# Kernel optimization log

Hardware: AMD Instinct MI355X
Metric: run time of the kernel (lower is better)

Reference implementation:

```python
import jax, jax.numpy as jnp
import numpy as np

N_NODES = 100000
N_EDGES = 2000000


def _init_mlp(key, dims, scale=0.05):
    Ws, bs = [], []
    ks = jax.random.split(key, len(dims) - 1)
    for k, di, do in zip(ks, dims[:-1], dims[1:]):
        Ws.append(jax.random.normal(k, (di, do), dtype=jnp.float32) * scale)
        bs.append(jnp.zeros((do,), dtype=jnp.float32))
    return Ws, bs


def setup_inputs() -> dict:
    key = jax.random.key(0)
    ks = jax.random.split(key, 7)
    d = {
        "t": jax.random.uniform(ks[0], (1,), dtype=jnp.float32),
        "x": jax.random.normal(ks[1], (N_NODES, 4), dtype=jnp.float32),
        "Ofixed": jax.random.normal(ks[2], (N_NODES, 2), dtype=jnp.float32),
        "src_idx": jax.random.randint(ks[3], (N_EDGES,), 0, N_NODES, dtype=jnp.int32),
        "tgt_idx": jax.random.randint(ks[4], (N_EDGES,), 0, N_NODES, dtype=jnp.int32),
    }
    # fR: (2*d_O+1)=13 -> [150]*4 -> 50 ; fO: 50 -> [100] -> 4
    R_Ws, R_bs = _init_mlp(ks[5], [13, 150, 150, 150, 150, 50])
    O_Ws, O_bs = _init_mlp(ks[6], [50, 100, 4])
    for i, (W, b) in enumerate(zip(R_Ws, R_bs)):
        d[f"fR_W{i}"] = W
        d[f"fR_b{i}"] = b
    for i, (W, b) in enumerate(zip(O_Ws, O_bs)):
        d[f"fO_W{i}"] = W
        d[f"fO_b{i}"] = b
    return d


def _mlp(h, Ws, bs):
    # hidden layers with ReLU, linear output (matches MLP in the torch code)
    for W, b in zip(Ws[:-1], bs[:-1]):
        h = jax.nn.relu(h @ W + b)
    return h @ Ws[-1] + bs[-1]


def reference(t, x, Ofixed, src_idx, tgt_idx,
              fR_W0, fR_b0, fR_W1, fR_b1, fR_W2, fR_b2, fR_W3, fR_b3, fR_W4, fR_b4,
              fO_W0, fO_b0, fO_W1, fO_b1):
    O = jnp.concatenate([x, Ofixed], axis=1)            # [N, d_O]
    # Msrc.T @ O and Mtgt.T @ O with 0/1 incidence matrices == gathers
    Rsrc = O[src_idx]                                   # [M, d_O]
    Rtgt = O[tgt_idx]                                   # [M, d_O]
    tt = jnp.broadcast_to(t.reshape(1, 1).astype(O.dtype), (src_idx.shape[0], 1))
    R_prime = jnp.concatenate([Rsrc, Rtgt, tt], axis=1)  # [M, 2*d_O+1]
    E = _mlp(R_prime, [fR_W0, fR_W1, fR_W2, fR_W3, fR_W4],
             [fR_b0, fR_b1, fR_b2, fR_b3, fR_b4])        # [M, d_E]
    # Mtgt @ E == scatter-add of edge messages onto target nodes
    E_prime = jax.ops.segment_sum(E, tgt_idx, num_segments=x.shape[0])  # [N, d_E]
    P = _mlp(E_prime, [fO_W0, fO_W1], [fO_b0, fO_b1])    # [N, d_P]
    return P
```

## Files before the change

### kernel.cpp

```cpp
#include <hip/hip_runtime.h>
#include <hip/hip_bf16.h>

typedef unsigned short u16;
typedef unsigned int u32;
typedef __attribute__((ext_vector_type(8))) short short8;
typedef __attribute__((ext_vector_type(4))) float f32x4;

constexpr int SA     = 160;
constexpr int BLK_E  = 128;
constexpr int NTHR   = 256;
constexpr int CHUNK  = 512;
constexpr int WSLOT  = 50 * CHUNK;
constexpr size_t WS_HDR   = 262144;

constexpr int Ls (int s) { return s == 0 ? 0 : (s <= 15 ? 1 + (s - 1) / 5 : 4); }
constexpr int Kss(int s) { return s == 0 ? 0 : (s <= 15 ? (s - 1) % 5 : s - 16); }

__device__ __forceinline__ u16 f2bf(float f) {
    union { float f; unsigned u; } c; c.f = f;
    return (u16)((c.u + 0x7fffu + ((c.u >> 16) & 1u)) >> 16);
}
__device__ __forceinline__ unsigned pk_bf16(float a, float b) {
    float2 f; f.x = a; f.y = b;
    __hip_bfloat162 h = __float22bfloat162_rn(f);
    return *(unsigned*)&h;
}

__device__ __forceinline__ int kperm(int kp) {
    if (kp < 64)  return (kp & 3) * 16 + (kp >> 2);
    if (kp < 128) { const int m = kp - 64; return (5 + (m & 3)) * 16 + (m >> 2); }
    if (kp < 144) return 4 * 16 + (kp - 128);
    if (kp < 160) return 9 * 16 + (kp - 144);
    return 1 << 30;
}

__global__ void prep_all(const float* __restrict__ W0, const float* __restrict__ W1,
                         const float* __restrict__ W2, const float* __restrict__ W3,
                         const float* __restrict__ W4,
                         const float* __restrict__ B0, const float* __restrict__ B1,
                         const float* __restrict__ B2, const float* __restrict__ B3,
                         const float* __restrict__ B4,
                         u16* __restrict__ Wt, u32* __restrict__ cursor, int n_nodes)
{
    const int l = blockIdx.y;
    if (l == 5) {
        for (int idx = blockIdx.x * blockDim.x + threadIdx.x; idx < n_nodes;
             idx += gridDim.x * blockDim.x)
            cursor[idx] = 0u;
        return;
    }
    const float* W; const float* B; int DI, DO; bool perm;
    if      (l == 0) { W = W0; B = B0; DI = 13;  DO = 150; perm = false; }
    else if (l == 1) { W = W1; B = B1; DI = 150; DO = 150; perm = true;  }
    else if (l == 2) { W = W2; B = B2; DI = 150; DO = 150; perm = true;  }
    else if (l == 3) { W = W3; B = B3; DI = 150; DO = 150; perm = true;  }
    else             { W = W4; B = B4; DI = 150; DO = 50;  perm = true;  }
    const int kbias = (l == 0) ? 13 : 150;
    u16* dst = Wt + (size_t)l * WSLOT;
    for (int idx = blockIdx.x * blockDim.x + threadIdx.x; idx < WSLOT;
         idx += gridDim.x * blockDim.x) {
        const int chunk = idx / CHUNK;
        const int within = idx - chunk * CHUNK;
        const int lane = within >> 3, e = within & 7;
        const int ks = chunk / 10, j = chunk - ks * 10;
        const int c = lane & 15, q = lane >> 4;
        const int n = j * 16 + c;
        const int kphys = ks * 32 + q * 8 + e;
        const int klog = perm ? kperm(kphys) : kphys;
        float v = 0.f;
        if (n < DO) {
            if (klog < DI)          v = W[klog * DO + n];
            else if (klog == kbias) v = B[n];
        }
        dst[idx] = f2bf(v);
    }
}

__device__ __forceinline__ void loadHalfH(const u16* __restrict__ Wt, int h,
                                          int lane, short8* buf)
{
    int l, ks, g, nch;
    if (h < 32) { const int s = h >> 1; l = Ls(s); ks = Kss(s); g = h & 1; nch = 5; }
    else        { l = 4; ks = h - 32; g = 0; nch = 4; }
    const u16* base = Wt + (size_t)l * WSLOT + (size_t)(ks * 10 + g * 5) * CHUNK
                         + lane * 8;
#pragma unroll
    for (int jj = 0; jj < 5; ++jj)
        if (jj < nch) buf[jj] = *(const short8*)&base[jj * CHUNK];
}

__device__ __forceinline__ void epilogueF(u16* act, int ebase, int col, int quad,
                                          f32x4 (&acc)[2][10])
{
#pragma unroll
    for (int mtl = 0; mtl < 2; ++mtl)
#pragma unroll
        for (int r = 0; r < 4; ++r) {
            const int row = ebase + mtl * 16 + quad * 4 + r;
            u16* rp = &act[row * SA];
            uint2 p0, p1;
            p0.x = pk_bf16(fmaxf(acc[mtl][0][r], 0.f), fmaxf(acc[mtl][1][r], 0.f));
            p0.y = pk_bf16(fmaxf(acc[mtl][2][r], 0.f), fmaxf(acc[mtl][3][r], 0.f));
            p1.x = pk_bf16(fmaxf(acc[mtl][5][r], 0.f), fmaxf(acc[mtl][6][r], 0.f));
            p1.y = pk_bf16(fmaxf(acc[mtl][7][r], 0.f), fmaxf(acc[mtl][8][r], 0.f));
            *(uint2*)&rp[col * 4]      = p0;
            *(uint2*)&rp[64 + col * 4] = p1;
            rp[128 + col] = (u16)pk_bf16(fmaxf(acc[mtl][4][r], 0.f), 0.f);
            u16 sv = (u16)pk_bf16(fmaxf(acc[mtl][9][r], 0.f), 0.f);
            if (col == 6) sv = 0x3F80;
            rp[144 + col] = sv;
        }
}

__global__ void hist_kernel(const int* __restrict__ tgt, u32* __restrict__ cnt,
                            int n_edges)
{
    const int e = blockIdx.x * blockDim.x + threadIdx.x;
    if (e < n_edges) atomicAdd(&cnt[tgt[e]], 1u);
}

__global__ void scan1_kernel(const u32* __restrict__ cnt, u32* __restrict__ offs,
                             u32* __restrict__ bsum, int n)
{
    __shared__ u32 s[256];
    const int i = blockIdx.x * 256 + threadIdx.x;
    const u32 v = (i < n) ? cnt[i] : 0u;
    s[threadIdx.x] = v; __syncthreads();
#pragma unroll
    for (int d = 1; d < 256; d <<= 1) {
        const u32 t = (threadIdx.x >= d) ? s[threadIdx.x - d] : 0u;
        __syncthreads();
        s[threadIdx.x] += t;
        __syncthreads();
    }
    if (i < n) offs[i] = s[threadIdx.x] - v;
    if (threadIdx.x == 255) bsum[blockIdx.x] = s[255];
}

__global__ void scan2_kernel(u32* __restrict__ bsum, int nb)
{
    __shared__ u32 s[512];
    const int i = threadIdx.x;
    const u32 v = (i < nb) ? bsum[i] : 0u;
    s[i] = v; __syncthreads();
#pragma unroll
    for (int d = 1; d < 512; d <<= 1) {
        const u32 t = (i >= d) ? s[i - d] : 0u;
        __syncthreads();
        s[i] += t;
        __syncthreads();
    }
    if (i < nb) bsum[i] = s[i] - v;
}

__global__ void scan3_kernel(u32* __restrict__ offs, const u32* __restrict__ bsum,
                             u32* __restrict__ cursor, int n, int n_edges)
{
    const int i = blockIdx.x * 256 + threadIdx.x;
    if (i < n) {
        const u32 o = offs[i] + bsum[blockIdx.x];
        offs[i] = o;
        cursor[i] = o;
    }
    if (blockIdx.x == 0 && threadIdx.x == 0) offs[n] = (u32)n_edges;
}

__global__ void perm_kernel(const int* __restrict__ src, const int* __restrict__ tgt,
                            u32* __restrict__ cursor, int2* __restrict__ sg,
                            int n_edges)
{
    const int e = blockIdx.x * blockDim.x + threadIdx.x;
    if (e < n_edges) {
        const int g = tgt[e];
        const u32 pos = atomicAdd(&cursor[g], 1u);
        sg[pos] = make_int2(src[e], g);
    }
}

__global__ __launch_bounds__(NTHR, 3) void edge_kernel(
    const float* __restrict__ t, const float* __restrict__ x, const float* __restrict__ Ofx,
    const int2* __restrict__ sgp,
    const u16* __restrict__ Wt,
    float* __restrict__ Ep, int n_edges)
{
    __shared__ __align__(16) u16 act[BLK_E * SA];

    const int tid   = threadIdx.x;
    const int lane  = tid & 63;
    const int wv    = tid >> 6;
    const int ebase = wv * 32;
    const int col   = lane & 15;
    const int quad  = lane >> 4;

    int gval = -1;
    if (lane < 32) {
        const int e = ebase + lane;
        const long long ge = (long long)blockIdx.x * BLK_E + e;
        const bool valid = ge < n_edges;
        const int2 sg = valid ? sgp[ge] : make_int2(0, 0);
        gval = valid ? sg.y : -1;
        const float4 xs = valid ? *(const float4*)&x[(size_t)sg.x * 4] : float4{0, 0, 0, 0};
        const float2 os = valid ? *(const float2*)&Ofx[(size_t)sg.x * 2] : float2{0, 0};
        const float4 xg = valid ? *(const float4*)&x[(size_t)sg.y * 4] : float4{0, 0, 0, 0};
        const float2 og = valid ? *(const float2*)&Ofx[(size_t)sg.y * 2] : float2{0, 0};
        const float tv = valid ? t[0] : 0.f;
        uint4 w0, w1;
        w0.x = pk_bf16(xs.x, xs.y); w0.y = pk_bf16(xs.z, xs.w);
        w0.z = pk_bf16(os.x, os.y); w0.w = pk_bf16(xg.x, xg.y);
        w1.x = pk_bf16(xg.z, xg.w); w1.y = pk_bf16(og.x, og.y);
        w1.z = pk_bf16(tv, 1.0f);   w1.w = 0u;
        u16* rp = &act[e * SA];
        *(uint4*)&rp[0]  = w0;
        *(uint4*)&rp[8]  = w1;
        *(uint4*)&rp[16] = uint4{0, 0, 0, 0};
        *(uint4*)&rp[24] = uint4{0, 0, 0, 0};
    }

    const f32x4 z = {0.f, 0.f, 0.f, 0.f};
    f32x4 acc[2][10];
    short8 Wb[2][5];
    short8 Af[2];

    loadHalfH(Wt, 0, lane, Wb[0]);
    loadHalfH(Wt, 1, lane, Wb[1]);

#pragma unroll
    for (int s = 0; s <= 15; ++s) {
        const int ks = Kss(s);
        const bool first = (s == 0) || (ks == 0);
#pragma unroll
        for (int mtl = 0; mtl < 2; ++mtl)
            Af[mtl] = *(const short8*)&act[(ebase + mtl * 16 + col) * SA
                                           + ks * 32 + quad * 8];
#pragma unroll
        for (int jj = 0; jj < 5; ++jj)
#pragma unroll
            for (int mtl = 0; mtl < 2; ++mtl)
                acc[mtl][jj] = __builtin_amdgcn_mfma_f32_16x16x32_bf16(
                    Af[mtl], Wb[0][jj], first ? z : acc[mtl][jj], 0, 0, 0);
        loadHalfH(Wt, 2 * s + 2, lane, Wb[0]);
#pragma unroll
        for (int jj = 0; jj < 5; ++jj)
#pragma unroll
            for (int mtl = 0; mtl < 2; ++mtl)
                acc[mtl][5 + jj] = __builtin_amdgcn_mfma_f32_16x16x32_bf16(
                    Af[mtl], Wb[1][jj], first ? z : acc[mtl][5 + jj], 0, 0, 0);
        loadHalfH(Wt, 2 * s + 3, lane, Wb[1]);
        if (s == 0 || ks == 4)
            epilogueF(act, ebase, col, quad, acc);
    }

    f32x4 acc4[2][4];
#pragma unroll
    for (int ks4 = 0; ks4 < 5; ++ks4) {
        const int h = 32 + ks4;
#pragma unroll
        for (int mtl = 0; mtl < 2; ++mtl)
            Af[mtl] = *(const short8*)&act[(ebase + mtl * 16 + col) * SA
                                           + ks4 * 32 + quad * 8];
#pragma unroll
        for (int jj = 0; jj < 4; ++jj)
#pragma unroll
            for (int mtl = 0; mtl < 2; ++mtl)
                acc4[mtl][jj] = __builtin_amdgcn_mfma_f32_16x16x32_bf16(
                    Af[mtl], Wb[h & 1][jj], (ks4 == 0) ? z : acc4[mtl][jj], 0, 0, 0);
        if (h + 2 <= 36) loadHalfH(Wt, h + 2, lane, Wb[h & 1]);
    }

    float* actF = (float*)&act[ebase * SA];
#pragma unroll
    for (int mtl = 0; mtl < 2; ++mtl)
#pragma unroll
        for (int jj = 0; jj < 4; ++jj) {
            const int n = jj * 16 + col;
            if (n < 50) {
#pragma unroll
                for (int r = 0; r < 4; ++r)
                    actF[(mtl * 16 + quad * 4 + r) * 52 + n] = acc4[mtl][jj][r];
            }
        }
    if (lane < 50) {
        const int c = lane;
        int   cur = __shfl(gval, 0);
        float a   = 0.f;
#pragma unroll
        for (int rb = 0; rb < 4; ++rb) {
            float vb[8];
#pragma unroll
            for (int j = 0; j < 8; ++j)
                vb[j] = actF[(rb * 8 + j) * 52 + c];
#pragma unroll
            for (int j = 0; j < 8; ++j) {
                const int g = __shfl(gval, rb * 8 + j);
                if (g != cur) {
                    if (cur >= 0) atomicAdd(&Ep[(size_t)cur * 50 + c], a);
                    a = 0.f; cur = g;
                }
                a += vb[j];
            }
        }
        if (cur >= 0) atomicAdd(&Ep[(size_t)cur * 50 + c], a);
    }
}

template<int DI, int DO, bool RELU>
__device__ __forceinline__ void mlp_layer_t(
    const float* __restrict__ W, const float* __restrict__ B,
    float (*in)[64], float (*out)[64], int tid)
{
    const int et = tid & 15;
    const int jt = tid >> 4;
    constexpr int NG = (DO + 15) / 16;

    float acc0[NG], acc1[NG], acc2[NG], acc3[NG];
#pragma unroll
    for (int g = 0; g < NG; ++g) {
        const int j = jt + 16 * g;
        const float bb = (j < DO) ? B[j] : 0.f;
        acc0[g] = bb; acc1[g] = bb; acc2[g] = bb; acc3[g] = bb;
    }
    for (int k = 0; k < DI; ++k) {
        const float4 a = *(const float4*)&in[k][et * 4];
#pragma unroll
        for (int g = 0; g < NG; ++g) {
            const int j = jt + 16 * g;
            const float wv = (j < DO) ? W[k * DO + j] : 0.f;
            acc0[g] = fmaf(a.x, wv, acc0[g]);
            acc1[g] = fmaf(a.y, wv, acc1[g]);
            acc2[g] = fmaf(a.z, wv, acc2[g]);
            acc3[g] = fmaf(a.w, wv, acc3[g]);
        }
    }
#pragma unroll
    for (int g = 0; g < NG; ++g) {
        const int j = jt + 16 * g;
        if (j < DO) {
            float4 v; v.x = acc0[g]; v.y = acc1[g]; v.z = acc2[g]; v.w = acc3[g];
            if (RELU) {
                v.x = fmaxf(v.x, 0.f); v.y = fmaxf(v.y, 0.f);
                v.z = fmaxf(v.z, 0.f); v.w = fmaxf(v.w, 0.f);
            }
            *(float4*)&out[j][et * 4] = v;
        }
    }
}

__global__ __launch_bounds__(256, 2) void node_kernel(
    const float* __restrict__ Ep,
    const float* __restrict__ W0, const float* __restrict__ B0,
    const float* __restrict__ W1, const float* __restrict__ B1,
    float* __restrict__ P, int n_nodes)
{
    __shared__ float bufA[104][64];
    __shared__ float bufB[104][64];
    const int tid = threadIdx.x;
    const int n0  = blockIdx.x * 64;

    for (int idx = tid; idx < 64 * 50; idx += 256) {
        const int e = idx / 50;
        const int k = idx - e * 50;
        const int n = n0 + e;
        bufA[k][e] = (n < n_nodes) ? Ep[(size_t)n * 50 + k] : 0.f;
    }
    __syncthreads();
    mlp_layer_t<50, 100, true >(W0, B0, bufA, bufB, tid); __syncthreads();
    mlp_layer_t<100, 4, false>(W1, B1, bufB, bufA, tid); __syncthreads();
    for (int idx = tid; idx < 64 * 4; idx += 256) {
        const int e = idx & 63;
        const int j = idx >> 6;
        const int n = n0 + e;
        if (n < n_nodes) P[(size_t)n * 4 + j] = bufA[j][e];
    }
}

extern "C" void kernel_launch(void* const* d_in, const int* in_sizes, int n_in,
                              void* d_out, int out_size, void* d_ws, size_t ws_size,
                              hipStream_t stream)
{
    const float* t   = (const float*)d_in[0];
    const float* x   = (const float*)d_in[1];
    const float* Ofx = (const float*)d_in[2];
    const int*   src = (const int*)d_in[3];
    const int*   tgt = (const int*)d_in[4];
    const float* W0  = (const float*)d_in[5];  const float* B0 = (const float*)d_in[6];
    const float* W1  = (const float*)d_in[7];  const float* B1 = (const float*)d_in[8];
    const float* W2  = (const float*)d_in[9];  const float* B2 = (const float*)d_in[10];
    const float* W3  = (const float*)d_in[11]; const float* B3 = (const float*)d_in[12];
    const float* W4  = (const float*)d_in[13]; const float* B4 = (const float*)d_in[14];
    const float* OW0 = (const float*)d_in[15]; const float* OB0 = (const float*)d_in[16];
    const float* OW1 = (const float*)d_in[17]; const float* OB1 = (const float*)d_in[18];

    const int n_nodes = in_sizes[1] / 4;
    const int n_edges = in_sizes[3];

    auto align256 = [](size_t v) { return (v + 255) & ~(size_t)255; };
    char* ws = (char*)d_ws;
    const size_t copy_elems = (size_t)n_nodes * 50;
    size_t o = 0;
    u16*   Wt       = (u16*)(ws + o);  o = WS_HDR;
    float* Ep       = (float*)(ws + o); o = align256(o + copy_elems * sizeof(float));
    u32*   offs     = (u32*)(ws + o);  o = align256(o + (size_t)(n_nodes + 1) * 4);
    u32*   cursor   = (u32*)(ws + o);  o = align256(o + (size_t)n_nodes * 4);
    u32*   bsum     = (u32*)(ws + o);  o = align256(o + 512 * 4);
    int2*  sg_perm  = (int2*)(ws + o); o = align256(o + (size_t)n_edges * 8);

    const int NB  = (n_nodes + 255) / 256;
    const int EBK = (n_edges + 255) / 256;

    prep_all<<<dim3(32, 6), 256, 0, stream>>>(W0, W1, W2, W3, W4,
                                              B0, B1, B2, B3, B4, Wt,
                                              cursor, n_nodes);
    hipMemsetAsync(Ep, 0, copy_elems * sizeof(float), stream);

    hist_kernel <<<EBK, 256, 0, stream>>>(tgt, cursor, n_edges);
    scan1_kernel<<<NB, 256, 0, stream>>>(cursor, offs, bsum, n_nodes);
    scan2_kernel<<<1, 512, 0, stream>>>(bsum, NB);
    scan3_kernel<<<NB, 256, 0, stream>>>(offs, bsum, cursor, n_nodes, n_edges);
    perm_kernel <<<EBK, 256, 0, stream>>>(src, tgt, cursor, sg_perm, n_edges);

    edge_kernel<<<(n_edges + BLK_E - 1) / BLK_E, NTHR, 0, stream>>>(
        t, x, Ofx, sg_perm, Wt, Ep, n_edges);

    node_kernel<<<(n_nodes + 63) / 64, 256, 0, stream>>>(
        Ep, OW0, OB0, OW1, OB1, (float*)d_out, n_nodes);
}
```

Baseline: 881.2 us.

## Fuse counting-sort kernels into one cooperative kernel and remap edge blocks per XCD

Replaces the histogram, three scan kernels and the permutation kernel with a single cooperative kernel that uses grid-wide syncs between phases. It also folds the Ep zeroing memset into the prep kernel, remaps edge-kernel block indices so consecutive edge blocks land on the same XCD for L2 locality, and raises node_kernel's occupancy hint. The aim is to cut launch overhead and improve cache reuse. The cooperative launch needs all NB (~391) blocks resident at once, and each grid.sync adds cost.

```diff
diff --git a/kernel.cpp b/kernel.cpp
--- a/kernel.cpp
+++ b/kernel.cpp
@@ -1,5 +1,8 @@
 #include <hip/hip_runtime.h>
 #include <hip/hip_bf16.h>
+#include <hip/hip_cooperative_groups.h>
+
+namespace cg = cooperative_groups;
 
 typedef unsigned short u16;
 typedef unsigned int u32;
@@ -40,13 +43,20 @@
                          const float* __restrict__ B0, const float* __restrict__ B1,
                          const float* __restrict__ B2, const float* __restrict__ B3,
                          const float* __restrict__ B4,
-                         u16* __restrict__ Wt, u32* __restrict__ cursor, int n_nodes)
+                         u16* __restrict__ Wt, u32* __restrict__ cursor, int n_nodes,
+                         float* __restrict__ Ep, int ep_quads)
 {
     const int l = blockIdx.y;
+    const int tid0 = blockIdx.x * blockDim.x + threadIdx.x;
+    const int stride = gridDim.x * blockDim.x;
     if (l == 5) {
-        for (int idx = blockIdx.x * blockDim.x + threadIdx.x; idx < n_nodes;
-             idx += gridDim.x * blockDim.x)
-            cursor[idx] = 0u;
+        for (int idx = tid0; idx < n_nodes; idx += stride) cursor[idx] = 0u;
+        return;
+    }
+    if (l == 6) {
+        float4* p = (float4*)Ep;
+        const float4 z4 = {0.f, 0.f, 0.f, 0.f};
+        for (int idx = tid0; idx < ep_quads; idx += stride) p[idx] = z4;
         return;
     }
     const float* W; const float* B; int DI, DO; bool perm;
@@ -57,8 +67,7 @@
     else             { W = W4; B = B4; DI = 150; DO = 50;  perm = true;  }
     const int kbias = (l == 0) ? 13 : 150;
     u16* dst = Wt + (size_t)l * WSLOT;
-    for (int idx = blockIdx.x * blockDim.x + threadIdx.x; idx < WSLOT;
-         idx += gridDim.x * blockDim.x) {
+    for (int idx = tid0; idx < WSLOT; idx += stride) {
         const int chunk = idx / CHUNK;
         const int within = idx - chunk * CHUNK;
         const int lane = within >> 3, e = within & 7;
@@ -112,65 +121,73 @@
         }
 }
 
-__global__ void hist_kernel(const int* __restrict__ tgt, u32* __restrict__ cnt,
-                            int n_edges)
-{
-    const int e = blockIdx.x * blockDim.x + threadIdx.x;
-    if (e < n_edges) atomicAdd(&cnt[tgt[e]], 1u);
-}
-
-__global__ void scan1_kernel(const u32* __restrict__ cnt, u32* __restrict__ offs,
-                             u32* __restrict__ bsum, int n)
-{
+__global__ void sort_coop(const int* __restrict__ src, const int* __restrict__ tgt,
+                          u32* __restrict__ cursor, u32* __restrict__ offs,
+                          u32* __restrict__ bsum, int2* __restrict__ sg,
+                          int n_nodes, int n_edges)
+{
+    cg::grid_group grid = cg::this_grid();
     __shared__ u32 s[256];
-    const int i = blockIdx.x * 256 + threadIdx.x;
-    const u32 v = (i < n) ? cnt[i] : 0u;
-    s[threadIdx.x] = v; __syncthreads();
-#pragma unroll
-    for (int d = 1; d < 256; d <<= 1) {
-        const u32 t = (threadIdx.x >= d) ? s[threadIdx.x - d] : 0u;
+    const int tid = threadIdx.x;
+    const int gstride = gridDim.x * blockDim.x;
+
+    for (int e = blockIdx.x * 256 + tid; e < n_edges; e += gstride)
+        atomicAdd(&cursor[tgt[e]], 1u);
+    grid.sync();
+
+    {
+        const int i = blockIdx.x * 256 + tid;
+        const u32 v = (i < n_nodes) ? cursor[i] : 0u;
+        s[tid] = v; __syncthreads();
+#pragma unroll
+        for (int d = 1; d < 256; d <<= 1) {
+            const u32 t2 = (tid >= d) ? s[tid - d] : 0u;
+            __syncthreads();
+            s[tid] += t2;
+            __syncthreads();
+        }
+        if (i < n_nodes) offs[i] = s[tid] - v;
+        if (tid == 255) bsum[blockIdx.x] = s[255];
+    }
+    grid.sync();
+
+    if (blockIdx.x == 0) {
+        const int nb = gridDim.x;
+        const u32 a = (tid < nb) ? bsum[tid] : 0u;
+        const u32 b = (tid + 256 < nb) ? bsum[tid + 256] : 0u;
+        s[tid] = a; __syncthreads();
+#pragma unroll
+        for (int d = 1; d < 256; d <<= 1) {
+            const u32 t2 = (tid >= d) ? s[tid - d] : 0u;
+            __syncthreads(); s[tid] += t2; __syncthreads();
+        }
+        const u32 ea = s[tid] - a;
+        const u32 atot = s[255];
         __syncthreads();
-        s[threadIdx.x] += t;
-        __syncthreads();
-    }
-    if (i < n) offs[i] = s[threadIdx.x] - v;
-    if (threadIdx.x == 255) bsum[blockIdx.x] = s[255];
-}
-
-__global__ void scan2_kernel(u32* __restrict__ bsum, int nb)
-{
-    __shared__ u32 s[512];
-    const int i = threadIdx.x;
-    const u32 v = (i < nb) ? bsum[i] : 0u;
-    s[i] = v; __syncthreads();
-#pragma unroll
-    for (int d = 1; d < 512; d <<= 1) {
-        const u32 t = (i >= d) ? s[i - d] : 0u;
-        __syncthreads();
-        s[i] += t;
-        __syncthreads();
-    }
-    if (i < nb) bsum[i] = s[i] - v;
-}
-
-__global__ void scan3_kernel(u32* __restrict__ offs, const u32* __restrict__ bsum,
-                             u32* __restrict__ cursor, int n, int n_edges)
-{
-    const int i = blockIdx.x * 256 + threadIdx.x;
-    if (i < n) {
-        const u32 o = offs[i] + bsum[blockIdx.x];
-        offs[i] = o;
-        cursor[i] = o;
-    }
-    if (blockIdx.x == 0 && threadIdx.x == 0) offs[n] = (u32)n_edges;
-}
-
-__global__ void perm_kernel(const int* __restrict__ src, const int* __restrict__ tgt,
-                            u32* __restrict__ cursor, int2* __restrict__ sg,
-                            int n_edges)
-{
-    const int e = blockIdx.x * blockDim.x + threadIdx.x;
-    if (e < n_edges) {
+        s[tid] = b; __syncthreads();
+#pragma unroll
+        for (int d = 1; d < 256; d <<= 1) {
+            const u32 t2 = (tid >= d) ? s[tid - d] : 0u;
+            __syncthreads(); s[tid] += t2; __syncthreads();
+        }
+        const u32 eb = atot + s[tid] - b;
+        if (tid < nb) bsum[tid] = ea;
+        if (tid + 256 < nb) bsum[tid + 256] = eb;
+    }
+    grid.sync();
+
+    {
+        const int i = blockIdx.x * 256 + tid;
+        if (i < n_nodes) {
+            const u32 o = offs[i] + bsum[blockIdx.x];
+            offs[i] = o;
+            cursor[i] = o;
+        }
+        if (blockIdx.x == 0 && tid == 0) offs[n_nodes] = (u32)n_edges;
+    }
+    grid.sync();
+
+    for (int e = blockIdx.x * 256 + tid; e < n_edges; e += gstride) {
         const int g = tgt[e];
         const u32 pos = atomicAdd(&cursor[g], 1u);
         sg[pos] = make_int2(src[e], g);
@@ -184,6 +201,13 @@
     float* __restrict__ Ep, int n_edges)
 {
     __shared__ __align__(16) u16 act[BLK_E * SA];
+
+    const int nwg  = gridDim.x;
+    const int orig = blockIdx.x;
+    const int xcd  = orig & 7;
+    const int q = nwg >> 3, r = nwg & 7;
+    const int bid = (xcd < r ? xcd * (q + 1) : r * (q + 1) + (xcd - r) * q)
+                    + (orig >> 3);
 
     const int tid   = threadIdx.x;
     const int lane  = tid & 63;
@@ -195,7 +219,7 @@
     int gval = -1;
     if (lane < 32) {
         const int e = ebase + lane;
-        const long long ge = (long long)blockIdx.x * BLK_E + e;
+        const long long ge = (long long)bid * BLK_E + e;
         const bool valid = ge < n_edges;
         const int2 sg = valid ? sgp[ge] : make_int2(0, 0);
         gval = valid ? sg.y : -1;
@@ -345,7 +369,7 @@
     }
 }
 
-__global__ __launch_bounds__(256, 2) void node_kernel(
+__global__ __launch_bounds__(256, 3) void node_kernel(
     const float* __restrict__ Ep,
     const float* __restrict__ W0, const float* __restrict__ B0,
     const float* __restrict__ W1, const float* __restrict__ B1,
@@ -404,19 +428,20 @@
     u32*   bsum     = (u32*)(ws + o);  o = align256(o + 512 * 4);
     int2*  sg_perm  = (int2*)(ws + o); o = align256(o + (size_t)n_edges * 8);
 
-    const int NB  = (n_nodes + 255) / 256;
-    const int EBK = (n_edges + 255) / 256;
-
-    prep_all<<<dim3(32, 6), 256, 0, stream>>>(W0, W1, W2, W3, W4,
+    const int NB = (n_nodes + 255) / 256;
+    const int ep_quads = (int)(copy_elems / 4);
+
+    prep_all<<<dim3(64, 7), 256, 0, stream>>>(W0, W1, W2, W3, W4,
                                               B0, B1, B2, B3, B4, Wt,
-                                              cursor, n_nodes);
-    hipMemsetAsync(Ep, 0, copy_elems * sizeof(float), stream);
-
-    hist_kernel <<<EBK, 256, 0, stream>>>(tgt, cursor, n_edges);
-    scan1_kernel<<<NB, 256, 0, stream>>>(cursor, offs, bsum, n_nodes);
-    scan2_kernel<<<1, 512, 0, stream>>>(bsum, NB);
-    scan3_kernel<<<NB, 256, 0, stream>>>(offs, bsum, cursor, n_nodes, n_edges);
-    perm_kernel <<<EBK, 256, 0, stream>>>(src, tgt, cursor, sg_perm, n_edges);
+                                              cursor, n_nodes, Ep, ep_quads);
+
+    {
+        void* cargs[] = {(void*)&src, (void*)&tgt, (void*)&cursor, (void*)&offs,
+                         (void*)&bsum, (void*)&sg_perm,
+                         (void*)&n_nodes, (void*)&n_edges};
+        hipLaunchCooperativeKernel((const void*)sort_coop, dim3(NB), dim3(256),
+                                   cargs, 0, stream);
+    }
 
     edge_kernel<<<(n_edges + BLK_E - 1) / BLK_E, NTHR, 0, stream>>>(
         t, x, Ofx, sg_perm, Wt, Ep, n_edges);
```

Result: slower. 1.069 ms (+21.3%).
